# Performance work log

Hardware: AMD Instinct MI355X
Metric: run time of the kernel (lower is better)

Reference implementation:

```python
import jax, jax.numpy as jnp
import numpy as np

NUM_Y_STEPS = 10
NUM_TYPES = 3
ANCHOR_DIM = 3 * NUM_Y_STEPS + 1  # 31
EPS = 1e-9


def setup_inputs() -> dict:
    key = jax.random.key(0)
    k1, k2, k3, k4, k5, k6 = jax.random.split(key, 6)
    B, A = 8192, 26
    D = NUM_TYPES * ANCHOR_DIM  # 93
    pred = jax.random.uniform(k1, (B, A, D), dtype=jnp.float32)
    gt = jax.random.uniform(k2, (B, A, D), dtype=jnp.float32)
    pred_hcam = jax.random.uniform(k3, (B,), dtype=jnp.float32) + 1.0
    gt_hcam = jax.random.uniform(k4, (B,), dtype=jnp.float32) + 1.0
    pred_pitch = jax.random.normal(k5, (B,), dtype=jnp.float32)
    gt_pitch = jax.random.normal(k6, (B,), dtype=jnp.float32)
    return {
        'pred_3D_lanes': pred,
        'gt_3D_lanes': gt,
        'pred_hcam': pred_hcam,
        'gt_hcam': gt_hcam,
        'pred_pitch': pred_pitch,
        'gt_pitch': gt_pitch,
    }


def reference(pred_3D_lanes, gt_3D_lanes, pred_hcam, gt_hcam, pred_pitch, gt_pitch):
    B, A, _ = pred_3D_lanes.shape
    K = NUM_Y_STEPS
    pred = pred_3D_lanes.reshape(B, A, NUM_TYPES, ANCHOR_DIM)
    gt = gt_3D_lanes.reshape(B, A, NUM_TYPES, ANCHOR_DIM)

    pred_class = pred[..., -1:]                # [B,A,T,1]
    pred_anchors = pred[..., : 2 * K]          # [B,A,T,2K]
    pred_vis = pred[..., 2 * K : 3 * K]        # [B,A,T,K]
    gt_class = gt[..., -1:]
    gt_anchors = gt[..., : 2 * K]
    gt_vis = gt[..., 2 * K : 3 * K]

    # loss0: binary cross entropy on visibility (note: (1-gt+eps) as in original)
    loss0 = -jnp.sum(
        gt_vis * jnp.log(pred_vis + EPS)
        + (1.0 - gt_vis + EPS) * jnp.log(1.0 - pred_vis + EPS)
    ) / K

    # loss1: binary cross entropy on lane class probability
    loss1 = -jnp.sum(
        gt_class * jnp.log(pred_class + EPS)
        + (1.0 - gt_class) * jnp.log(1.0 - pred_class + EPS)
    )

    # loss2: visibility/class-masked L1 on X-offset and Z anchors
    vis2 = jnp.concatenate([gt_vis, gt_vis], axis=3)  # [B,A,T,2K]
    loss2 = jnp.sum(jnp.abs(gt_class * vis2 * (pred_anchors - gt_anchors)))

    total = loss0 + loss1 + loss2
    return (total, loss0, loss1, loss2)
```

## Files before the change

kernel.cpp:

```cpp
#include <hip/hip_runtime.h>

#define EPSL 1e-9f
#define TFLOATS 1984
#define NTILES 9984
#define NBLOCKS 1248
#define WPB 2
#define NWAVES (NBLOCKS * WPB)
#define NT 4
#define NSLOTS 64


__global__ __launch_bounds__(128) void laneline_reduce_kernel(
    const float* __restrict__ pred,
    const float* __restrict__ gt,
    float* __restrict__ ws)
{
    __shared__ __align__(16) float sp[WPB][TFLOATS];
    __shared__ __align__(16) float sg[WPB][TFLOATS];

    const int lane = threadIdx.x & 63;
    const int wid  = threadIdx.x >> 6;
    const int wg   = blockIdx.x * WPB + wid;
    const bool full = (lane < 48);

    float4 pa0,pa1,pa2,pa3,pa4,pa5,pa6,pa7;
    float4 ga0,ga1,ga2,ga3,ga4,ga5,ga6,ga7;
    float4 pb0,pb1,pb2,pb3,pb4,pb5,pb6,pb7;
    float4 gb0,gb1,gb2,gb3,gb4,gb5,gb6,gb7;

#define LOADT(p,g,tile) do{ \
    const float4* gp_ = (const float4*)(pred + (size_t)(tile) * TFLOATS) + lane; \
    const float4* gg_ = (const float4*)(gt   + (size_t)(tile) * TFLOATS) + lane; \
    p##0 = gp_[0];   p##1 = gp_[64];  p##2 = gp_[128]; p##3 = gp_[192]; \
    p##4 = gp_[256]; p##5 = gp_[320]; p##6 = gp_[384]; \
    g##0 = gg_[0];   g##1 = gg_[64];  g##2 = gg_[128]; g##3 = gg_[192]; \
    g##4 = gg_[256]; g##5 = gg_[320]; g##6 = gg_[384]; \
    if (full) { p##7 = gp_[448]; g##7 = gg_[448]; } \
}while(0)

#define STORET(p,g) do{ \
    float4* dp_ = (float4*)&sp[wid][0] + lane; \
    float4* dg_ = (float4*)&sg[wid][0] + lane; \
    dp_[0]   = p##0; dp_[64]  = p##1; dp_[128] = p##2; dp_[192] = p##3; \
    dp_[256] = p##4; dp_[320] = p##5; dp_[384] = p##6; \
    dg_[0]   = g##0; dg_[64]  = g##1; dg_[128] = g##2; dg_[192] = g##3; \
    dg_[256] = g##4; dg_[320] = g##5; dg_[384] = g##6; \
    if (full) { dp_[448] = p##7; dg_[448] = g##7; } \
}while(0)

    float s0 = 0.f, s1 = 0.f, s2 = 0.f;

#define COMPUTE() do{ \
    const float* lp = &sp[wid][lane * 31]; \
    const float* lg = &sg[wid][lane * 31]; \
    const float gcls = lg[30]; \
    _Pragma("unroll") \
    for (int i = 0; i < 10; ++i) { \
        const float gvis = lg[20 + i]; \
         \
        s2 += gcls * gvis * (fabsf(lp[i]      - lg[i]) \
                           + fabsf(lp[10 + i] - lg[10 + i])); \
        const float pv = lp[20 + i]; \
        s0 += gvis * __logf(pv + EPSL) \
            + (1.0f - gvis + EPSL) * __logf(1.0f - pv + EPSL); \
    } \
    const float pc = lp[30]; \
    s1 += gcls * __logf(pc + EPSL) \
        + (1.0f - gcls) * __logf(1.0f - pc + EPSL); \
}while(0)

    LOADT(pa,ga, wg);
    LOADT(pb,gb, wg + NWAVES);

    STORET(pa,ga);
    LOADT(pa,ga, wg + 2*NWAVES);
    COMPUTE();

    STORET(pb,gb);
    LOADT(pb,gb, wg + 3*NWAVES);
    COMPUTE();

    STORET(pa,ga);
    COMPUTE();

    STORET(pb,gb);
    COMPUTE();

#undef LOADT
#undef STORET
#undef COMPUTE

#pragma unroll
    for (int off = 32; off > 0; off >>= 1) {
        s0 += __shfl_down(s0, off, 64);
        s1 += __shfl_down(s1, off, 64);
        s2 += __shfl_down(s2, off, 64);
    }
    if (lane == 0) {
        float* slot = ws + (wg & (NSLOTS - 1)) * 16;
        atomicAdd(&slot[0], s0);
        atomicAdd(&slot[1], s1);
        atomicAdd(&slot[2], s2);
    }
}

__global__ __launch_bounds__(64) void laneline_finalize_kernel(
    const float* __restrict__ ws, float* __restrict__ out)
{
    const int t = threadIdx.x;
    float v0 = ws[t * 16], v1 = ws[t * 16 + 1], v2 = ws[t * 16 + 2];
#pragma unroll
    for (int off = 32; off > 0; off >>= 1) {
        v0 += __shfl_down(v0, off, 64);
        v1 += __shfl_down(v1, off, 64);
        v2 += __shfl_down(v2, off, 64);
    }
    if (t == 0) {
        const float l0 = -v0 * 0.1f;
        const float l1 = -v1;
        const float l2 =  v2;
        out[0] = l0 + l1 + l2;
        out[1] = l0;
        out[2] = l1;
        out[3] = l2;
    }
}

extern "C" void kernel_launch(void* const* d_in, const int* in_sizes, int n_in,
                              void* d_out, int out_size, void* d_ws, size_t ws_size,
                              hipStream_t stream)
{
    const float* pred = (const float*)d_in[0];
    const float* gt   = (const float*)d_in[1];
    float* ws  = (float*)d_ws;
    float* out = (float*)d_out;

    hipMemsetAsync(ws, 0, NSLOTS * 16 * sizeof(float), stream);

    laneline_reduce_kernel<<<NBLOCKS, 128, 0, stream>>>(pred, gt, ws);
    laneline_finalize_kernel<<<1, 64, 0, stream>>>(ws, out);
}
```

Before: 192.0 us.

## Replace LDS-staged tiles with direct per-thread aligned float4 group loads

Drops the shared-memory staging of 64-group tiles. Each thread now reads its own 31-float groups straight from global memory with aligned float4 loads, and the branch on thread index mod 4 picks the alignment offset. This removes the LDS round trip and the software double-buffering. The cost is strided, non-coalesced per-thread global accesses (124-byte stride) and some redundant bytes loaded, plus divergent code paths inside each wave.

```diff
diff --git a/kernel.cpp b/kernel.cpp
--- a/kernel.cpp
+++ b/kernel.cpp
@@ -1,94 +1,59 @@
 #include <hip/hip_runtime.h>
 
 #define EPSL 1e-9f
-#define TFLOATS 1984
-#define NTILES 9984
-#define NBLOCKS 1248
-#define WPB 2
-#define NWAVES (NBLOCKS * WPB)
-#define NT 4
+#define NG 638976
+#define GPT 3
+#define TTHREADS (NG / GPT)
+#define NBLOCKS (TTHREADS / 256)
 #define NSLOTS 64
 
 
-__global__ __launch_bounds__(128) void laneline_reduce_kernel(
+#define C4(v, c) ((c) == 0 ? (v).x : (c) == 1 ? (v).y : (c) == 2 ? (v).z : (v).w)
+
+__global__ __launch_bounds__(256) void laneline_reduce_kernel(
     const float* __restrict__ pred,
     const float* __restrict__ gt,
     float* __restrict__ ws)
 {
-    __shared__ __align__(16) float sp[WPB][TFLOATS];
-    __shared__ __align__(16) float sg[WPB][TFLOATS];
-
-    const int lane = threadIdx.x & 63;
-    const int wid  = threadIdx.x >> 6;
-    const int wg   = blockIdx.x * WPB + wid;
-    const bool full = (lane < 48);
-
-    float4 pa0,pa1,pa2,pa3,pa4,pa5,pa6,pa7;
-    float4 ga0,ga1,ga2,ga3,ga4,ga5,ga6,ga7;
-    float4 pb0,pb1,pb2,pb3,pb4,pb5,pb6,pb7;
-    float4 gb0,gb1,gb2,gb3,gb4,gb5,gb6,gb7;
-
-#define LOADT(p,g,tile) do{ \
-    const float4* gp_ = (const float4*)(pred + (size_t)(tile) * TFLOATS) + lane; \
-    const float4* gg_ = (const float4*)(gt   + (size_t)(tile) * TFLOATS) + lane; \
-    p##0 = gp_[0];   p##1 = gp_[64];  p##2 = gp_[128]; p##3 = gp_[192]; \
-    p##4 = gp_[256]; p##5 = gp_[320]; p##6 = gp_[384]; \
-    g##0 = gg_[0];   g##1 = gg_[64];  g##2 = gg_[128]; g##3 = gg_[192]; \
-    g##4 = gg_[256]; g##5 = gg_[320]; g##6 = gg_[384]; \
-    if (full) { p##7 = gp_[448]; g##7 = gg_[448]; } \
-}while(0)
-
-#define STORET(p,g) do{ \
-    float4* dp_ = (float4*)&sp[wid][0] + lane; \
-    float4* dg_ = (float4*)&sg[wid][0] + lane; \
-    dp_[0]   = p##0; dp_[64]  = p##1; dp_[128] = p##2; dp_[192] = p##3; \
-    dp_[256] = p##4; dp_[320] = p##5; dp_[384] = p##6; \
-    dg_[0]   = g##0; dg_[64]  = g##1; dg_[128] = g##2; dg_[192] = g##3; \
-    dg_[256] = g##4; dg_[320] = g##5; dg_[384] = g##6; \
-    if (full) { dp_[448] = p##7; dg_[448] = g##7; } \
-}while(0)
-
+    const int gtid = blockIdx.x * 256 + threadIdx.x;
     float s0 = 0.f, s1 = 0.f, s2 = 0.f;
 
-#define COMPUTE() do{ \
-    const float* lp = &sp[wid][lane * 31]; \
-    const float* lg = &sg[wid][lane * 31]; \
-    const float gcls = lg[30]; \
+#define BODY(R, NQ) do { \
     _Pragma("unroll") \
-    for (int i = 0; i < 10; ++i) { \
-        const float gvis = lg[20 + i]; \
-         \
-        s2 += gcls * gvis * (fabsf(lp[i]      - lg[i]) \
-                           + fabsf(lp[10 + i] - lg[10 + i])); \
-        const float pv = lp[20 + i]; \
-        s0 += gvis * __logf(pv + EPSL) \
-            + (1.0f - gvis + EPSL) * __logf(1.0f - pv + EPSL); \
+    for (int k = 0; k < GPT; ++k) { \
+        const size_t g = (size_t)gtid + (size_t)k * TTHREADS; \
+        const float4* P4 = (const float4*)(pred + (g * 31 - (R))); \
+        const float4* G4 = (const float4*)(gt   + (g * 31 - (R))); \
+        float4 qp[NQ], qg[NQ]; \
+        _Pragma("unroll") \
+        for (int q = 0; q < (NQ); ++q) { qp[q] = P4[q]; qg[q] = G4[q]; } \
+        const float gcls = C4(qg[((R) + 30) >> 2], ((R) + 30) & 3); \
+        _Pragma("unroll") \
+        for (int i = 0; i < 10; ++i) { \
+            const float gvis = C4(qg[((R) + 20 + i) >> 2], ((R) + 20 + i) & 3); \
+             \
+            s2 += gcls * gvis * ( \
+                  fabsf(C4(qp[((R) + i) >> 2], ((R) + i) & 3) \
+                      - C4(qg[((R) + i) >> 2], ((R) + i) & 3)) \
+                + fabsf(C4(qp[((R) + 10 + i) >> 2], ((R) + 10 + i) & 3) \
+                      - C4(qg[((R) + 10 + i) >> 2], ((R) + 10 + i) & 3))); \
+            const float pv = C4(qp[((R) + 20 + i) >> 2], ((R) + 20 + i) & 3); \
+            s0 += gvis * __logf(pv + EPSL) \
+                + (1.0f - gvis + EPSL) * __logf(1.0f - pv + EPSL); \
+        } \
+        const float pc = C4(qp[((R) + 30) >> 2], ((R) + 30) & 3); \
+        s1 += gcls * __logf(pc + EPSL) \
+            + (1.0f - gcls) * __logf(1.0f - pc + EPSL); \
     } \
-    const float pc = lp[30]; \
-    s1 += gcls * __logf(pc + EPSL) \
-        + (1.0f - gcls) * __logf(1.0f - pc + EPSL); \
-}while(0)
+} while (0)
 
-    LOADT(pa,ga, wg);
-    LOADT(pb,gb, wg + NWAVES);
+    const int rsel = threadIdx.x & 3;
+    if      (rsel == 0) BODY(0, 8);
+    else if (rsel == 1) BODY(3, 9);
+    else if (rsel == 2) BODY(2, 9);
+    else                BODY(1, 8);
 
-    STORET(pa,ga);
-    LOADT(pa,ga, wg + 2*NWAVES);
-    COMPUTE();
-
-    STORET(pb,gb);
-    LOADT(pb,gb, wg + 3*NWAVES);
-    COMPUTE();
-
-    STORET(pa,ga);
-    COMPUTE();
-
-    STORET(pb,gb);
-    COMPUTE();
-
-#undef LOADT
-#undef STORET
-#undef COMPUTE
+#undef BODY
 
 #pragma unroll
     for (int off = 32; off > 0; off >>= 1) {
@@ -96,8 +61,8 @@
         s1 += __shfl_down(s1, off, 64);
         s2 += __shfl_down(s2, off, 64);
     }
-    if (lane == 0) {
-        float* slot = ws + (wg & (NSLOTS - 1)) * 16;
+    if ((threadIdx.x & 63) == 0) {
+        float* slot = ws + ((gtid >> 6) & (NSLOTS - 1)) * 16;
         atomicAdd(&slot[0], s0);
         atomicAdd(&slot[1], s1);
         atomicAdd(&slot[2], s2);
@@ -137,6 +102,6 @@
 
     hipMemsetAsync(ws, 0, NSLOTS * 16 * sizeof(float), stream);
 
-    laneline_reduce_kernel<<<NBLOCKS, 128, 0, stream>>>(pred, gt, ws);
+    laneline_reduce_kernel<<<NBLOCKS, 256, 0, stream>>>(pred, gt, ws);
     laneline_finalize_kernel<<<1, 64, 0, stream>>>(ws, out);
 }
```

Result: slower. 208.6 us (+8.6%).
